# Performance work log

Measured on AMD Instinct MI355X. Metric: run time of the kernel, lower is better.

## Reference

```python
import jax, jax.numpy as jnp
import numpy as np

N_NODES = 100000
N_EDGES = 1600000
D = 64


def setup_inputs() -> dict:
    key = jax.random.key(0)
    k0, k1, k2, k3 = jax.random.split(key, 4)
    scale = 1.0 / np.sqrt(D)
    return {
        "x": jax.random.normal(k0, (N_NODES, D), dtype=jnp.float32),
        "W1": jax.random.normal(k1, (D, D), dtype=jnp.float32) * scale,
        "W2": jax.random.normal(k2, (D, D), dtype=jnp.float32) * scale,
        "b2": jnp.zeros((D,), dtype=jnp.float32),
        "edge_index": jax.random.randint(k3, (2, N_EDGES), 0, N_NODES, dtype=jnp.int32),
    }


def reference(x, W1, W2, b2, edge_index):
    # KapoorConv forward in eval mode (Dropout(p=0.5) is identity at inference).
    n = x.shape[0]
    # GCNConv adds self-loops, then symmetric normalization D^-1/2 A D^-1/2.
    loops = jnp.arange(n, dtype=edge_index.dtype)
    src = jnp.concatenate([edge_index[0], loops])  # message source j
    dst = jnp.concatenate([edge_index[1], loops])  # aggregation target i
    deg = jnp.zeros((n,), x.dtype).at[dst].add(jnp.float32(1.0))
    dinv = jax.lax.rsqrt(deg)  # deg >= 1 thanks to self-loops
    norm = (dinv[src] * dinv[dst])[:, None]  # [E+N, 1]

    def gcn(h, W, b):
        h = h @ W                                   # dense transform first
        msg = h[src] * norm                         # gather + normalize
        out = jax.ops.segment_sum(msg, dst, num_segments=n)  # scatter-add
        return out if b is None else out + b

    h = jax.nn.relu(gcn(x, W1, None))  # layer1: bias=False
    return gcn(h, W2, b2)              # layer2: bias=True
```

## Files before the change

kernel.cpp:

```cpp
#include <hip/hip_runtime.h>

#define D 64
#define CHUNK 8192
#define BKT_SHIFT 8
#define BKT_NODES 256
#define MAXB 512
#define CAP 8192
#define GROWS 64
#define SSTR 68

typedef unsigned int u32;

__device__ __forceinline__ u32 bfr(float v) {
    u32 x = __float_as_uint(v);
    return (x + 0x7fffu + ((x >> 16) & 1u)) >> 16;
}
__device__ __forceinline__ u32 pack2(float lo, float hi) { return bfr(lo) | (bfr(hi) << 16); }
__device__ __forceinline__ float blo(u32 w) { return __uint_as_float(w << 16); }
__device__ __forceinline__ float bhi(u32 w) { return __uint_as_float(w & 0xffff0000u); }


__global__ void init_cursor(int* __restrict__ cursor, int B) {
    int i = blockIdx.x * blockDim.x + threadIdx.x;
    if (i < B) cursor[i] = i * CAP;
}


__global__ void partition(const int* __restrict__ src, const int* __restrict__ dst,
                          int* __restrict__ cursor, int* __restrict__ packed,
                          int nE, int B) {
    __shared__ int hist[MAXB];
    __shared__ int delta[MAXB];
    __shared__ int s[MAXB];
    __shared__ int sorted[CHUNK];
    __shared__ unsigned short sortedb[CHUNK];
    int t = threadIdx.x;
    int i0 = blockIdx.x * CHUNK;
    int cn = min(CHUNK, nE - i0);

    hist[t] = 0;
    __syncthreads();
    for (int i = t; i < cn; i += 512) atomicAdd(&hist[dst[i0 + i] >> BKT_SHIFT], 1);
    __syncthreads();

    int v = hist[t];
    s[t] = v;
    __syncthreads();
    for (int off = 1; off < MAXB; off <<= 1) {
        int u = (t >= off) ? s[t - off] : 0;
        __syncthreads();
        s[t] += u;
        __syncthreads();
    }
    {
        int excl = s[t] - v;
        int rb = 0;
        if (t < B && v > 0) rb = atomicAdd(&cursor[t], v);
        delta[t] = rb - excl;
        hist[t] = excl;
    }
    __syncthreads();

    for (int i = t; i < cn; i += 512) {
        int d = dst[i0 + i];
        int b = d >> BKT_SHIFT;
        int pp = atomicAdd(&hist[b], 1);
        sorted[pp]  = ((d & (BKT_NODES - 1)) << 17) | src[i0 + i];
        sortedb[pp] = (unsigned short)b;
    }
    __syncthreads();

    for (int i = t; i < cn; i += 512) {
        packed[delta[sortedb[i]] + i] = sorted[i];
    }
}


__global__ void bucket_csr(const int* __restrict__ packed, const int* __restrict__ cursor,
                           int* __restrict__ row_ptr, float* __restrict__ dinv,
                           int* __restrict__ adj, const float* __restrict__ x,
                           u32* __restrict__ xp, int n, int B) {
    __shared__ int s[BKT_NODES];
    __shared__ int cur[BKT_NODES];
    __shared__ float dv[BKT_NODES];
    __shared__ int base_s;
    int t = threadIdx.x;
    int b = blockIdx.x;
    int rlo = b * CAP;
    int mycnt = min(cursor[b] - rlo, CAP);

    int partial = 0;
    for (int i = t; i < b; i += BKT_NODES) partial += cursor[i] - i * CAP;
    s[t] = partial;
    __syncthreads();
    for (int off = BKT_NODES / 2; off > 0; off >>= 1) {
        if (t < off) s[t] += s[t + off];
        __syncthreads();
    }
    if (t == 0) base_s = s[0];
    __syncthreads();
    int base = base_s;
    if (b == B - 1 && t == 0) row_ptr[n] = base + mycnt;

    s[t] = 0;
    __syncthreads();
    for (int i = t; i < mycnt; i += BKT_NODES) atomicAdd(&s[packed[rlo + i] >> 17], 1);
    __syncthreads();

    int v = s[t];
    __syncthreads();
    for (int off = 1; off < BKT_NODES; off <<= 1) {
        int u = (t >= off) ? s[t - off] : 0;
        __syncthreads();
        s[t] += u;
        __syncthreads();
    }
    int gbeg = base + s[t] - v;
    int node = (b << BKT_SHIFT) + t;
    float di = rsqrtf(1.0f + (float)v);
    if (node < n) {
        row_ptr[node] = gbeg;
        dinv[node] = di;
    }
    dv[t] = di;
    cur[t] = gbeg;
    __syncthreads();

    for (int i = t; i < mycnt; i += BKT_NODES) {
        int w = packed[rlo + i];
        int pos = atomicAdd(&cur[w >> 17], 1);
        adj[pos] = w & 0x1FFFF;
    }

    int nbase = b << BKT_SHIFT;
    for (int i = t; i < BKT_NODES * 8; i += BKT_NODES) {
        int row = i >> 3, fb = i & 7;
        int nd = nbase + row;
        if (nd < n) {
            float d2 = dv[row];
            const float4* xr = (const float4*)(x + (size_t)nd * D + 8 * fb);
            float4 v0 = xr[0], v1 = xr[1];
            uint4 w;
            w.x = pack2(d2 * v0.x, d2 * v0.y);
            w.y = pack2(d2 * v0.z, d2 * v0.w);
            w.z = pack2(d2 * v1.x, d2 * v1.y);
            w.w = pack2(d2 * v1.z, d2 * v1.w);
            ((uint4*)(xp + (size_t)nd * (D / 2)))[fb] = w;
        }
    }
}

__launch_bounds__(256, 4)
__global__ void agg(const u32* __restrict__ hp, const int* __restrict__ row_ptr,
                    const int* __restrict__ adj, float* __restrict__ S, int n) {
    const int lane = threadIdx.x & 63;
    const int o = lane >> 3;
    const int f = lane & 7;
    const int wave = (blockIdx.x * blockDim.x + threadIdx.x) >> 6;
    const int nw = (gridDim.x * blockDim.x) >> 6;

    for (int nb = wave * 8; nb < n; nb += nw * 8) {
        int nq = nb + o;
        bool valid = nq < n;
        int nqc = valid ? nq : 0;
        int rb = row_ptr[nqc];
        int re = row_ptr[nqc + 1];
        int len = valid ? (re - rb) : 0;

        uint4 sw = ((const uint4*)(hp + (size_t)nqc * (D / 2)))[f];
        float acc[8];
        acc[0] = blo(sw.x); acc[1] = bhi(sw.x);
        acc[2] = blo(sw.y); acc[3] = bhi(sw.y);
        acc[4] = blo(sw.z); acc[5] = bhi(sw.z);
        acc[6] = blo(sw.w); acc[7] = bhi(sw.w);

        int lm = len;
        lm = max(lm, __shfl_xor(lm, 8, 64));
        lm = max(lm, __shfl_xor(lm, 16, 64));
        lm = max(lm, __shfl_xor(lm, 32, 64));

        for (int base = 0; base < lm; base += 8) {
            int rem = len - base;
            int idx_l = 0;
            if (f < rem) idx_l = adj[rb + base + f];
            int ss[8]; uint4 vv[8];
#pragma unroll
            for (int u = 0; u < 8; ++u) {
                ss[u] = __shfl(idx_l, (o << 3) | u, 64);
            }
#pragma unroll
            for (int u = 0; u < 8; ++u) {
                vv[u] = ((const uint4*)(hp + (size_t)ss[u] * (D / 2)))[f];
            }
#pragma unroll
            for (int u = 0; u < 8; ++u) {
                float m = (u < rem) ? 1.0f : 0.0f;
                acc[0] = fmaf(m, blo(vv[u].x), acc[0]);
                acc[1] = fmaf(m, bhi(vv[u].x), acc[1]);
                acc[2] = fmaf(m, blo(vv[u].y), acc[2]);
                acc[3] = fmaf(m, bhi(vv[u].y), acc[3]);
                acc[4] = fmaf(m, blo(vv[u].z), acc[4]);
                acc[5] = fmaf(m, bhi(vv[u].z), acc[5]);
                acc[6] = fmaf(m, blo(vv[u].w), acc[6]);
                acc[7] = fmaf(m, bhi(vv[u].w), acc[7]);
            }
        }
        if (valid) {
            float4* sp = (float4*)(S + (size_t)nq * D + 8 * f);
            sp[0] = make_float4(acc[0], acc[1], acc[2], acc[3]);
            sp[1] = make_float4(acc[4], acc[5], acc[6], acc[7]);
        }
    }
}

template <int MODE>
__launch_bounds__(256, 4)
__global__ void tgemm(const float* __restrict__ S, const float* __restrict__ W,
                      const float* __restrict__ bias, const float* __restrict__ dinv,
                      float* __restrict__ outf, u32* __restrict__ outb, int n) {
    __shared__ float Wl[D * D];
    __shared__ float Sl[GROWS * SSTR];
    const int t = threadIdx.x;

    for (int i = t; i < D * D / 4; i += 256)
        ((float4*)Wl)[i] = ((const float4*)W)[i];

    const int R0 = blockIdx.x * GROWS;
    for (int i = t; i < GROWS * 16; i += 256) {
        int row = i >> 4, kq = i & 15;
        float4 v = make_float4(0.f, 0.f, 0.f, 0.f);
        if (R0 + row < n) v = ((const float4*)(S + (size_t)(R0 + row) * D))[kq];
        *(float4*)&Sl[row * SSTR + kq * 4] = v;
    }
    __syncthreads();

    const int cg = t & 15;
    const int rg = t >> 4;

    float4 acc0 = make_float4(0.f, 0.f, 0.f, 0.f);
    float4 acc1 = make_float4(0.f, 0.f, 0.f, 0.f);
    float4 acc2 = make_float4(0.f, 0.f, 0.f, 0.f);
    float4 acc3 = make_float4(0.f, 0.f, 0.f, 0.f);

#pragma unroll 4
    for (int k = 0; k < D; k += 4) {
        float4 a0 = *(const float4*)&Sl[(4 * rg + 0) * SSTR + k];
        float4 a1 = *(const float4*)&Sl[(4 * rg + 1) * SSTR + k];
        float4 a2 = *(const float4*)&Sl[(4 * rg + 2) * SSTR + k];
        float4 a3 = *(const float4*)&Sl[(4 * rg + 3) * SSTR + k];
        float4 w0 = *(const float4*)&Wl[(k + 0) * D + 4 * cg];
        float4 w1 = *(const float4*)&Wl[(k + 1) * D + 4 * cg];
        float4 w2 = *(const float4*)&Wl[(k + 2) * D + 4 * cg];
        float4 w3 = *(const float4*)&Wl[(k + 3) * D + 4 * cg];
#define MAC(ACC, A)                                                        \
        ACC.x = fmaf(A.x, w0.x, fmaf(A.y, w1.x, fmaf(A.z, w2.x, fmaf(A.w, w3.x, ACC.x)))); \
        ACC.y = fmaf(A.x, w0.y, fmaf(A.y, w1.y, fmaf(A.z, w2.y, fmaf(A.w, w3.y, ACC.y)))); \
        ACC.z = fmaf(A.x, w0.z, fmaf(A.y, w1.z, fmaf(A.z, w2.z, fmaf(A.w, w3.z, ACC.z)))); \
        ACC.w = fmaf(A.x, w0.w, fmaf(A.y, w1.w, fmaf(A.z, w2.w, fmaf(A.w, w3.w, ACC.w))))
        MAC(acc0, a0);
        MAC(acc1, a1);
        MAC(acc2, a2);
        MAC(acc3, a3);
#undef MAC
    }

    const float4 bv = (MODE == 1) ? ((const float4*)bias)[cg]
                                  : make_float4(0.f, 0.f, 0.f, 0.f);
    float4 accs[4] = {acc0, acc1, acc2, acc3};
#pragma unroll
    for (int r = 0; r < 4; ++r) {
        int row = R0 + 4 * rg + r;
        if (row >= n) break;
        float dn = dinv[row];
        float4 y = accs[r];
        if (MODE == 0) {
            float o0 = dn * fmaxf(dn * y.x, 0.f);
            float o1 = dn * fmaxf(dn * y.y, 0.f);
            float o2 = dn * fmaxf(dn * y.z, 0.f);
            float o3 = dn * fmaxf(dn * y.w, 0.f);
            uint2 w2o;
            w2o.x = pack2(o0, o1);
            w2o.y = pack2(o2, o3);
            ((uint2*)(outb + (size_t)row * (D / 2)))[cg] = w2o;
        } else {
            float4 o;
            o.x = fmaf(dn, y.x, bv.x);
            o.y = fmaf(dn, y.y, bv.y);
            o.z = fmaf(dn, y.z, bv.z);
            o.w = fmaf(dn, y.w, bv.w);
            ((float4*)(outf + (size_t)row * D))[cg] = o;
        }
    }
}


extern "C" void kernel_launch(void* const* d_in, const int* in_sizes, int n_in,
                              void* d_out, int out_size, void* d_ws, size_t ws_size,
                              hipStream_t stream) {
    const float* x  = (const float*)d_in[0];
    const float* W1 = (const float*)d_in[1];
    const float* W2 = (const float*)d_in[2];
    const float* b2 = (const float*)d_in[3];
    const int*   ei = (const int*)d_in[4];

    int n  = in_sizes[0] / D;
    int nE = in_sizes[4] / 2;
    const int* src = ei;
    const int* dst = ei + nE;

    int B = (n + BKT_NODES - 1) >> BKT_SHIFT;

    auto align = [](size_t v) { return (v + 255) & ~(size_t)255; };
    char* ws = (char*)d_ws;
    size_t off = 0;
    int* row_ptr = (int*)(ws + off);   off += align((size_t)(n + 1) * 4);
    float* dinv  = (float*)(ws + off); off += align((size_t)n * 4);
    int* cursor  = (int*)(ws + off);   off += align((size_t)MAXB * 4);
    int* adj     = (int*)(ws + off);   off += align((size_t)nE * 4);
    int* packed  = (int*)(ws + off);   off += align((size_t)(B + 1) * CAP * 4);
    u32* F0      = (u32*)(ws + off);   off += align((size_t)n * (D / 2) * 4);
    float* Sbuf  = (float*)(ws + off);
    float* out = (float*)d_out;

    int nchunks = (nE + CHUNK - 1) / CHUNK;

    init_cursor<<<2, 256, 0, stream>>>(cursor, B);
    partition<<<nchunks, 512, 0, stream>>>(src, dst, cursor, packed, nE, B);
    bucket_csr<<<B, BKT_NODES, 0, stream>>>(packed, cursor, row_ptr, dinv, adj, x, F0, n, B);

    int gblocks = (n + GROWS - 1) / GROWS;

    agg<<<1024, 256, 0, stream>>>(F0, row_ptr, adj, Sbuf, n);
    tgemm<0><<<gblocks, 256, 0, stream>>>(Sbuf, W1, nullptr, dinv, nullptr, F0, n);

    agg<<<1024, 256, 0, stream>>>(F0, row_ptr, adj, Sbuf, n);
    tgemm<1><<<gblocks, 256, 0, stream>>>(Sbuf, W2, b2, dinv, out, nullptr, n);
}
```

Measured before the change: 225.2 us.

## Fuse neighbor aggregation with dense transform into one kernel per layer

Merges the aggregation kernel and the tiled GEMM kernel so that each block aggregates its 64 rows straight into shared memory and then multiplies by W. This removes the fp32 intermediate S write and reread through global memory and drops two launches. A separate bf16 buffer F1 is used because layer one can no longer write back into F0 while other blocks still read it. In exchange, aggregation moves from a grid-stride loop over 1024 blocks to a fixed 64-row-per-block mapping, and each block reloads W into shared memory, which may hurt load balance and latency hiding.

After: 205.7 us. 1.09x faster.

```diff
diff --git a/kernel.cpp b/kernel.cpp
--- a/kernel.cpp
+++ b/kernel.cpp
@@ -150,17 +150,31 @@
     }
 }
 
+template <int MODE>
 __launch_bounds__(256, 4)
-__global__ void agg(const u32* __restrict__ hp, const int* __restrict__ row_ptr,
-                    const int* __restrict__ adj, float* __restrict__ S, int n) {
-    const int lane = threadIdx.x & 63;
+__global__ void fused(const u32* __restrict__ hp, const int* __restrict__ row_ptr,
+                      const int* __restrict__ adj,
+                      const float* __restrict__ W, const float* __restrict__ bias,
+                      const float* __restrict__ dinv,
+                      float* __restrict__ outf, u32* __restrict__ outb, int n) {
+    __shared__ float Wl[D * D];
+    __shared__ float Sl[GROWS * SSTR];
+    const int t = threadIdx.x;
+
+    for (int i = t; i < D * D / 4; i += 256)
+        ((float4*)Wl)[i] = ((const float4*)W)[i];
+
+    const int R0 = blockIdx.x * GROWS;
+
+    const int lane = t & 63;
     const int o = lane >> 3;
     const int f = lane & 7;
-    const int wave = (blockIdx.x * blockDim.x + threadIdx.x) >> 6;
-    const int nw = (gridDim.x * blockDim.x) >> 6;
-
-    for (int nb = wave * 8; nb < n; nb += nw * 8) {
-        int nq = nb + o;
+    const int wv = t >> 6;
+
+#pragma unroll
+    for (int r = 0; r < 2; ++r) {
+        int row = wv * 16 + r * 8 + o;
+        int nq = R0 + row;
         bool valid = nq < n;
         int nqc = valid ? nq : 0;
         int rb = row_ptr[nqc];
@@ -205,32 +219,8 @@
                 acc[7] = fmaf(m, bhi(vv[u].w), acc[7]);
             }
         }
-        if (valid) {
-            float4* sp = (float4*)(S + (size_t)nq * D + 8 * f);
-            sp[0] = make_float4(acc[0], acc[1], acc[2], acc[3]);
-            sp[1] = make_float4(acc[4], acc[5], acc[6], acc[7]);
-        }
-    }
-}
-
-template <int MODE>
-__launch_bounds__(256, 4)
-__global__ void tgemm(const float* __restrict__ S, const float* __restrict__ W,
-                      const float* __restrict__ bias, const float* __restrict__ dinv,
-                      float* __restrict__ outf, u32* __restrict__ outb, int n) {
-    __shared__ float Wl[D * D];
-    __shared__ float Sl[GROWS * SSTR];
-    const int t = threadIdx.x;
-
-    for (int i = t; i < D * D / 4; i += 256)
-        ((float4*)Wl)[i] = ((const float4*)W)[i];
-
-    const int R0 = blockIdx.x * GROWS;
-    for (int i = t; i < GROWS * 16; i += 256) {
-        int row = i >> 4, kq = i & 15;
-        float4 v = make_float4(0.f, 0.f, 0.f, 0.f);
-        if (R0 + row < n) v = ((const float4*)(S + (size_t)(R0 + row) * D))[kq];
-        *(float4*)&Sl[row * SSTR + kq * 4] = v;
+        *(float4*)&Sl[row * SSTR + 8 * f]     = make_float4(acc[0], acc[1], acc[2], acc[3]);
+        *(float4*)&Sl[row * SSTR + 8 * f + 4] = make_float4(acc[4], acc[5], acc[6], acc[7]);
     }
     __syncthreads();
 
@@ -283,12 +273,12 @@
             w2o.y = pack2(o2, o3);
             ((uint2*)(outb + (size_t)row * (D / 2)))[cg] = w2o;
         } else {
-            float4 o;
-            o.x = fmaf(dn, y.x, bv.x);
-            o.y = fmaf(dn, y.y, bv.y);
-            o.z = fmaf(dn, y.z, bv.z);
-            o.w = fmaf(dn, y.w, bv.w);
-            ((float4*)(outf + (size_t)row * D))[cg] = o;
+            float4 oo;
+            oo.x = fmaf(dn, y.x, bv.x);
+            oo.y = fmaf(dn, y.y, bv.y);
+            oo.z = fmaf(dn, y.z, bv.z);
+            oo.w = fmaf(dn, y.w, bv.w);
+            ((float4*)(outf + (size_t)row * D))[cg] = oo;
         }
     }
 }
@@ -319,7 +309,7 @@
     int* adj     = (int*)(ws + off);   off += align((size_t)nE * 4);
     int* packed  = (int*)(ws + off);   off += align((size_t)(B + 1) * CAP * 4);
     u32* F0      = (u32*)(ws + off);   off += align((size_t)n * (D / 2) * 4);
-    float* Sbuf  = (float*)(ws + off);
+    u32* F1      = (u32*)(ws + off);
     float* out = (float*)d_out;
 
     int nchunks = (nE + CHUNK - 1) / CHUNK;
@@ -330,9 +320,7 @@
 
     int gblocks = (n + GROWS - 1) / GROWS;
 
-    agg<<<1024, 256, 0, stream>>>(F0, row_ptr, adj, Sbuf, n);
-    tgemm<0><<<gblocks, 256, 0, stream>>>(Sbuf, W1, nullptr, dinv, nullptr, F0, n);
-
-    agg<<<1024, 256, 0, stream>>>(F0, row_ptr, adj, Sbuf, n);
-    tgemm<1><<<gblocks, 256, 0, stream>>>(Sbuf, W2, b2, dinv, out, nullptr, n);
-}
+    fused<0><<<gblocks, 256, 0, stream>>>(F0, row_ptr, adj, W1, nullptr, dinv, nullptr, F1, n);
+
+    fused<1><<<gblocks, 256, 0, stream>>>(F1, row_ptr, adj, W2, b2, dinv, out, nullptr, n);
+}
```
